# Kernel tuning notes

Measured on AMD Instinct MI355X. Metric: run time of the kernel, lower is better.

Reference implementation:

```python
import jax, jax.numpy as jnp
import numpy as np

FDIM = 512
NUM_HEADS = 8
FATT = FDIM // NUM_HEADS  # 64


def setup_inputs() -> dict:
    key = jax.random.key(0)
    ks = jax.random.split(key, 8)
    Nx, Np = 2048, 4096
    s = 0.05
    return {
        "fx_in": jax.random.normal(ks[0], (Nx, FDIM), jnp.float32),
        "fp_in": jax.random.normal(ks[1], (1, Np, FDIM), jnp.float32),
        "Wembd": jax.random.normal(ks[2], (NUM_HEADS, FATT, FDIM), jnp.float32) * s,
        "bembd": jax.random.normal(ks[3], (NUM_HEADS, FATT), jnp.float32) * s,
        "Wfc": jax.random.normal(ks[4], (NUM_HEADS, FATT, 2 * FATT), jnp.float32) * s,
        "bfc": jax.random.normal(ks[5], (NUM_HEADS, FATT), jnp.float32) * s,
        "Wout": jax.random.normal(ks[6], (FDIM, FATT * NUM_HEADS), jnp.float32) * s,
        "bout": jax.random.normal(ks[7], (FDIM,), jnp.float32) * s,
    }


def reference(fx_in, fp_in, Wembd, bembd, Wfc, bfc, Wout, bout):
    # fx_in: [Nx, F]; fp_in: [1, Np, F] -> squeeze leading dim
    fp0 = fp_in[0]
    Nx = fx_in.shape[0]
    d = jnp.sqrt(jnp.asarray(FATT, fx_in.dtype))
    # per-head embedding of concatenated [fx; fp]: [H, Nx+Np, e]
    f = jnp.concatenate([fx_in, fp0], axis=0)
    femb = jnp.einsum('nf,hef->hne', f, Wembd) + bembd[:, None, :]
    fx, fp = femb[:, :Nx], femb[:, Nx:]          # [H,Nx,e], [H,Np,e]
    # attention weights (dropout is identity in eval)
    scores = jnp.einsum('hxe,hpe->hxp', fx, fp) / d
    w = jax.nn.softmax(scores, axis=2)            # [H,Nx,Np]
    # gather + concat + per-head fuse MLP
    fa_att = jnp.einsum('hxp,hpe->hxe', w, fp)    # [H,Nx,e]
    fa = jnp.concatenate([fa_att, fx], axis=2)    # [H,Nx,2e]
    fa = jax.nn.relu(jnp.einsum('hxc,hec->hxe', fa, Wfc) + bfc[:, None, :])
    fa = jnp.transpose(fa, (1, 0, 2)).reshape(Nx, -1)  # [Nx, H*e]
    fx_out = jax.nn.relu(fx_in + fa @ Wout.T + bout)
    w_out = jnp.transpose(w, (1, 0, 2))           # [Nx, H, Np]
    return fx_out, w_out
```

## Files before the change

### kernel.cpp

```cpp
#include <hip/hip_runtime.h>

typedef unsigned short ushort_t;
using frag_ab = __attribute__((ext_vector_type(8))) short;
using f32x4   = __attribute__((ext_vector_type(4))) float;
using u32x4   = __attribute__((ext_vector_type(4))) unsigned int;
using u32x2   = __attribute__((ext_vector_type(2))) unsigned int;

#define FDIM 512
#define NH 8
#define FATT 64
#define NX 2048
#define NP 4096
#define NTOT 6144

__device__ __forceinline__ ushort_t f2bf(float f) {
    unsigned u = __float_as_uint(f);
    u = (u + 0x7FFFu + ((u >> 16) & 1u)) >> 16;
    return (ushort_t)u;
}
__device__ __forceinline__ float bf2f(ushort_t s) {
    return __uint_as_float(((unsigned)s) << 16);
}
__device__ __forceinline__ unsigned pk2bf(float a, float b) {
    return (unsigned)f2bf(a) | ((unsigned)f2bf(b) << 16);
}

__global__ __launch_bounds__(256) void k_prep(const float* __restrict__ fx,
                                              const float* __restrict__ fp,
                                              const float* __restrict__ We,
                                              const float* __restrict__ Wfc,
                                              const float* __restrict__ Wout,
                                              ushort_t* __restrict__ f_b,
                                              ushort_t* __restrict__ We_b,
                                              ushort_t* __restrict__ Wfc_b,
                                              ushort_t* __restrict__ Wout_b) {
    int i = blockIdx.x * 256 + threadIdx.x;
    int stride = gridDim.x * 256;
    const int NF4 = NTOT * FDIM / 4;
    const int NX4 = NX * FDIM / 4;
    for (int idx = i; idx < NF4; idx += stride) {
        float4 v = (idx < NX4) ? ((const float4*)fx)[idx]
                               : ((const float4*)fp)[idx - NX4];
        ushort4 o;
        o.x = f2bf(v.x); o.y = f2bf(v.y); o.z = f2bf(v.z); o.w = f2bf(v.w);
        ((ushort4*)f_b)[idx] = o;
    }
    const int NW4 = FDIM * FDIM / 4;
    for (int idx = i; idx < NW4; idx += stride) {
        float4 v = ((const float4*)We)[idx];
        ushort4 o;
        o.x = f2bf(v.x); o.y = f2bf(v.y); o.z = f2bf(v.z); o.w = f2bf(v.w);
        ((ushort4*)We_b)[idx] = o;
    }
    const int NFC4 = NH * FATT * 2 * FATT / 4;
    for (int idx = i; idx < NFC4; idx += stride) {
        float4 v = ((const float4*)Wfc)[idx];
        ushort4 o;
        o.x = f2bf(v.x); o.y = f2bf(v.y); o.z = f2bf(v.z); o.w = f2bf(v.w);
        ((ushort4*)Wfc_b)[idx] = o;
    }
    for (int idx = i; idx < NW4; idx += stride) {
        float4 v = ((const float4*)Wout)[idx];
        ushort4 o;
        o.x = f2bf(v.x); o.y = f2bf(v.y); o.z = f2bf(v.z); o.w = f2bf(v.w);
        ((ushort4*)Wout_b)[idx] = o;
    }
}

__global__ __launch_bounds__(256) void k_embed(const ushort_t* __restrict__ f_b,
                                               const ushort_t* __restrict__ We_b,
                                               const float* __restrict__ bembd,
                                               ushort_t* __restrict__ femb_b,
                                               ushort_t* __restrict__ fpT_b,
                                               ushort_t* __restrict__ facat_b) {
    int tid = threadIdx.x;
    int wv = tid >> 6, lane = tid & 63;
    int g = lane >> 4, c = lane & 15;
    int m0 = blockIdx.x * 64 + wv * 16;
    int o0 = blockIdx.y * 64;

    f32x4 acc[4] = {};
    const ushort_t* arow = f_b + (size_t)(m0 + c) * FDIM + g * 8;
#pragma unroll 4
    for (int ks = 0; ks < FDIM; ks += 32) {
        frag_ab a = *(const frag_ab*)(arow + ks);
#pragma unroll
        for (int t = 0; t < 4; ++t) {
            const ushort_t* brow = We_b + (size_t)(o0 + t * 16 + c) * FDIM + ks + g * 8;
            frag_ab b = *(const frag_ab*)brow;
            acc[t] = __builtin_amdgcn_mfma_f32_16x16x32_bf16(a, b, acc[t], 0, 0, 0);
        }
    }
#pragma unroll
    for (int t = 0; t < 4; ++t) {
        int o = o0 + t * 16 + c;
        int h = o >> 6, e = o & 63;
        float bia = bembd[o];
#pragma unroll
        for (int r = 0; r < 4; ++r) {
            int n = m0 + g * 4 + r;
            ushort_t v = f2bf(acc[t][r] + bia);
            femb_b[((size_t)h * NTOT + n) * FATT + e] = v;
            if (n >= NX) fpT_b[((size_t)h * FATT + e) * NP + (n - NX)] = v;
            else         facat_b[((size_t)h * NX + n) * 128 + 64 + e] = v;
        }
    }
}

__global__ __launch_bounds__(512) void k_attn_p1(const ushort_t* __restrict__ femb_b,
                                                 const ushort_t* __restrict__ fpT_b,
                                                 float* __restrict__ inv_sums,
                                                 ushort_t* __restrict__ facat_b) {
    int bid = blockIdx.x;
    int h  = bid & 7;
    int xb = bid >> 3;
    int tid = threadIdx.x;
    int wv = tid >> 6;
    int lane = tid & 63;
    int g = lane >> 4, c = lane & 15;

    __shared__ float lds_pv[64][68];
    __shared__ float lds_sum[64];
    __shared__ float lds_inv[64];

    const ushort_t* fxb = femb_b + (size_t)h * NTOT * FATT;
    const ushort_t* fpb = fxb + (size_t)NX * FATT;
    const ushort_t* fTb = fpT_b + (size_t)h * FATT * NP;

    frag_ab bx0_0, bx0_1, bx1_0, bx1_1, bx2_0, bx2_1, bx3_0, bx3_1;
    {
        const ushort_t* b0 = fxb + (size_t)(xb * 64 + 0 * 16 + c) * FATT + g * 8;
        const ushort_t* b1 = fxb + (size_t)(xb * 64 + 1 * 16 + c) * FATT + g * 8;
        const ushort_t* b2 = fxb + (size_t)(xb * 64 + 2 * 16 + c) * FATT + g * 8;
        const ushort_t* b3 = fxb + (size_t)(xb * 64 + 3 * 16 + c) * FATT + g * 8;
        bx0_0 = *(const frag_ab*)b0;  bx0_1 = *(const frag_ab*)(b0 + 32);
        bx1_0 = *(const frag_ab*)b1;  bx1_1 = *(const frag_ab*)(b1 + 32);
        bx2_0 = *(const frag_ab*)b2;  bx2_1 = *(const frag_ab*)(b2 + 32);
        bx3_0 = *(const frag_ab*)b3;  bx3_1 = *(const frag_ab*)(b3 + 32);
    }

    f32x4 pacc[4][4] = {};
    float rsum[4] = {0.f, 0.f, 0.f, 0.f};
    const int p0 = wv * 512;

    for (int ps = p0; ps < p0 + 512; ps += 16) {
        const ushort_t* ar = fpb + (size_t)(ps + c) * FATT + g * 8;
        frag_ab a0 = *(const frag_ab*)ar;
        frag_ab a1 = *(const frag_ab*)(ar + 32);
        frag_ab pb[4];
#pragma unroll
        for (int xg = 0; xg < 4; ++xg) {
            frag_ab q0 = (xg == 0) ? bx0_0 : (xg == 1) ? bx1_0 : (xg == 2) ? bx2_0 : bx3_0;
            frag_ab q1 = (xg == 0) ? bx0_1 : (xg == 1) ? bx1_1 : (xg == 2) ? bx2_1 : bx3_1;
            f32x4 s = {};
            s = __builtin_amdgcn_mfma_f32_16x16x32_bf16(a0, q0, s, 0, 0, 0);
            s = __builtin_amdgcn_mfma_f32_16x16x32_bf16(a1, q1, s, 0, 0, 0);
            float e0 = __expf(s[0] * 0.125f);
            float e1 = __expf(s[1] * 0.125f);
            float e2 = __expf(s[2] * 0.125f);
            float e3 = __expf(s[3] * 0.125f);
            rsum[xg] += (e0 + e1) + (e2 + e3);
            u32x4 bw;
            bw[0] = pk2bf(e0, e1);
            bw[1] = pk2bf(e2, e3);
            bw[2] = 0u;
            bw[3] = 0u;
            pb[xg] = __builtin_bit_cast(frag_ab, bw);
        }
#pragma unroll
        for (int t2 = 0; t2 < 4; ++t2) {
            const ushort_t* vr = fTb + (size_t)(t2 * 16 + c) * NP + ps + g * 4;
            u32x2 vl = *(const u32x2*)vr;
            u32x4 aw;
            aw[0] = vl[0];
            aw[1] = vl[1];
            aw[2] = 0u;
            aw[3] = 0u;
            frag_ab va = __builtin_bit_cast(frag_ab, aw);
#pragma unroll
            for (int xg = 0; xg < 4; ++xg)
                pacc[xg][t2] = __builtin_amdgcn_mfma_f32_16x16x32_bf16(va, pb[xg], pacc[xg][t2], 0, 0, 0);
        }
    }

#pragma unroll
    for (int xg = 0; xg < 4; ++xg) {
        rsum[xg] += __shfl_xor(rsum[xg], 16);
        rsum[xg] += __shfl_xor(rsum[xg], 32);
    }

    for (int w = 0; w < 8; ++w) {
        if (wv == w) {
            if (w == 0) {
                if (lane < 16) {
#pragma unroll
                    for (int xg = 0; xg < 4; ++xg) lds_sum[xg * 16 + c] = rsum[xg];
                }
#pragma unroll
                for (int xg = 0; xg < 4; ++xg)
#pragma unroll
                    for (int t2 = 0; t2 < 4; ++t2)
                        *(f32x4*)&lds_pv[xg * 16 + c][t2 * 16 + 4 * g] = pacc[xg][t2];
            } else {
                if (lane < 16) {
#pragma unroll
                    for (int xg = 0; xg < 4; ++xg) lds_sum[xg * 16 + c] += rsum[xg];
                }
#pragma unroll
                for (int xg = 0; xg < 4; ++xg)
#pragma unroll
                    for (int t2 = 0; t2 < 4; ++t2) {
                        f32x4 cur = *(const f32x4*)&lds_pv[xg * 16 + c][t2 * 16 + 4 * g];
                        cur += pacc[xg][t2];
                        *(f32x4*)&lds_pv[xg * 16 + c][t2 * 16 + 4 * g] = cur;
                    }
            }
        }
        __syncthreads();
    }
    if (tid < 64) {
        float inv = 1.f / lds_sum[tid];
        lds_inv[tid] = inv;
        inv_sums[(size_t)h * NX + xb * 64 + tid] = inv;
    }
    __syncthreads();

    {
        int row = tid >> 3;
        int e0 = (tid & 7) * 8;
        float inv = lds_inv[row];
        u32x4 o;
#pragma unroll
        for (int j = 0; j < 4; ++j)
            o[j] = pk2bf(lds_pv[row][e0 + 2 * j] * inv, lds_pv[row][e0 + 2 * j + 1] * inv);
        *(u32x4*)&facat_b[((size_t)h * NX + xb * 64 + row) * 128 + e0] = o;
    }
}

__global__ __launch_bounds__(256) void k_wout(const ushort_t* __restrict__ femb_b,
                                              const float* __restrict__ inv_sums,
                                              float* __restrict__ w_out) {
    int bid = blockIdx.x;
    int h  = bid & 7;
    int wv = threadIdx.x >> 6;
    int t1 = (bid >> 3) * 4 + wv;
    int xt = t1 & 127;
    int sl = t1 >> 7;
    int lane = threadIdx.x & 63;
    int g = lane >> 4, c = lane & 15;

    __shared__ float lds[4][16][132];

    const ushort_t* fxb = femb_b + (size_t)h * NTOT * FATT;
    const ushort_t* fpb = fxb + (size_t)NX * FATT;

    const ushort_t* brow = fxb + (size_t)(xt * 16 + c) * FATT + g * 8;
    frag_ab b0 = *(const frag_ab*)(brow);
    frag_ab b1 = *(const frag_ab*)(brow + 32);
    float inv_c = inv_sums[(size_t)h * NX + xt * 16 + c];

    const int p0 = sl * 512;
    for (int chunk = 0; chunk < 512; chunk += 128) {
#pragma unroll
        for (int pt = 0; pt < 8; ++pt) {
            int ps = p0 + chunk + pt * 16;
            const ushort_t* arow = fpb + (size_t)(ps + c) * FATT + g * 8;
            f32x4 s = {};
            s = __builtin_amdgcn_mfma_f32_16x16x32_bf16(*(const frag_ab*)arow, b0, s, 0, 0, 0);
            s = __builtin_amdgcn_mfma_f32_16x16x32_bf16(*(const frag_ab*)(arow + 32), b1, s, 0, 0, 0);
            f32x4 ev;
            ev[0] = __expf(s[0] * 0.125f) * inv_c;
            ev[1] = __expf(s[1] * 0.125f) * inv_c;
            ev[2] = __expf(s[2] * 0.125f) * inv_c;
            ev[3] = __expf(s[3] * 0.125f) * inv_c;
            int sw = (pt * 16 + g * 4) ^ ((c & 7) << 4);
            *(f32x4*)&lds[wv][c][sw] = ev;
        }
        __syncthreads();
#pragma unroll
        for (int row = 0; row < 16; ++row) {
            int pi = lane * 2;
            int swr = pi ^ ((row & 7) << 4);
            float2 v = *(const float2*)&lds[wv][row][swr];
            float* dst = w_out + ((size_t)(xt * 16 + row) * NH + h) * NP + p0 + chunk + pi;
            *(float2*)dst = v;
        }
        __syncthreads();
    }
}

__global__ __launch_bounds__(256) void k_fc(const ushort_t* __restrict__ facat_b,
                                            const ushort_t* __restrict__ Wfc_b,
                                            const float* __restrict__ bfc,
                                            ushort_t* __restrict__ fcout_b) {
    int tid = threadIdx.x;
    int wv = tid >> 6, lane = tid & 63;
    int g = lane >> 4, c = lane & 15;
    int x0 = blockIdx.x * 64 + wv * 16;
    int h = blockIdx.y;

    const ushort_t* A = facat_b + ((size_t)h * NX + x0 + c) * 128 + g * 8;
    const ushort_t* B = Wfc_b + (size_t)h * FATT * 128;

    f32x4 acc[4] = {};
#pragma unroll
    for (int ks = 0; ks < 128; ks += 32) {
        frag_ab a = *(const frag_ab*)(A + ks);
#pragma unroll
        for (int t = 0; t < 4; ++t) {
            frag_ab b = *(const frag_ab*)(B + (size_t)(t * 16 + c) * 128 + ks + g * 8);
            acc[t] = __builtin_amdgcn_mfma_f32_16x16x32_bf16(a, b, acc[t], 0, 0, 0);
        }
    }
#pragma unroll
    for (int t = 0; t < 4; ++t) {
        int e = t * 16 + c;
        float bia = bfc[h * FATT + e];
#pragma unroll
        for (int r = 0; r < 4; ++r) {
            int x = x0 + g * 4 + r;
            fcout_b[(size_t)x * FDIM + h * FATT + e] = f2bf(fmaxf(acc[t][r] + bia, 0.f));
        }
    }
}

__global__ __launch_bounds__(256) void k_out(const float* __restrict__ fx_in,
                                             const ushort_t* __restrict__ fcout_b,
                                             const ushort_t* __restrict__ Wout_b,
                                             const float* __restrict__ bout,
                                             float* __restrict__ out) {
    int tid = threadIdx.x;
    int wv = tid >> 6, lane = tid & 63;
    int g = lane >> 4, c = lane & 15;
    int x0 = blockIdx.x * 64 + wv * 16;
    int o0 = blockIdx.y * 64;

    f32x4 acc[4] = {};
    const ushort_t* A = fcout_b + (size_t)(x0 + c) * FDIM + g * 8;
#pragma unroll 4
    for (int ks = 0; ks < FDIM; ks += 32) {
        frag_ab a = *(const frag_ab*)(A + ks);
#pragma unroll
        for (int t = 0; t < 4; ++t) {
            frag_ab b = *(const frag_ab*)(Wout_b + (size_t)(o0 + t * 16 + c) * FDIM + ks + g * 8);
            acc[t] = __builtin_amdgcn_mfma_f32_16x16x32_bf16(a, b, acc[t], 0, 0, 0);
        }
    }
#pragma unroll
    for (int t = 0; t < 4; ++t) {
        int f = o0 + t * 16 + c;
        float bia = bout[f];
#pragma unroll
        for (int r = 0; r < 4; ++r) {
            int x = x0 + g * 4 + r;
            float v = acc[t][r] + bia + fx_in[(size_t)x * FDIM + f];
            out[(size_t)x * FDIM + f] = fmaxf(v, 0.f);
        }
    }
}

extern "C" void kernel_launch(void* const* d_in, const int* in_sizes, int n_in,
                              void* d_out, int out_size, void* d_ws, size_t ws_size,
                              hipStream_t stream) {
    const float* fx_in = (const float*)d_in[0];
    const float* fp_in = (const float*)d_in[1];
    const float* Wembd = (const float*)d_in[2];
    const float* bembd = (const float*)d_in[3];
    const float* Wfc   = (const float*)d_in[4];
    const float* bfc   = (const float*)d_in[5];
    const float* Wout  = (const float*)d_in[6];
    const float* bout  = (const float*)d_in[7];

    float* out   = (float*)d_out;
    float* w_out = out + (size_t)NX * FDIM;

    ushort_t* f_b     = (ushort_t*)d_ws;
    ushort_t* We_b    = f_b + (size_t)NTOT * FDIM;
    ushort_t* femb_b  = We_b + (size_t)FDIM * FDIM;
    ushort_t* fpT_b   = femb_b + (size_t)NH * NTOT * FATT;
    ushort_t* facat_b = fpT_b + (size_t)NH * FATT * NP;
    ushort_t* fcout_b = facat_b + (size_t)NH * NX * 128;
    ushort_t* Wfc_b   = fcout_b + (size_t)NX * FDIM;
    ushort_t* Wout_b  = Wfc_b + (size_t)NH * FATT * 2 * FATT;
    float*    inv_sums= (float*)(Wout_b + (size_t)FDIM * FDIM);

    k_prep   <<<1024, 256, 0, stream>>>(fx_in, fp_in, Wembd, Wfc, Wout,
                                        f_b, We_b, Wfc_b, Wout_b);
    k_embed  <<<dim3(96, 8), 256, 0, stream>>>(f_b, We_b, bembd, femb_b, fpT_b, facat_b);
    k_attn_p1<<<256, 512, 0, stream>>>(femb_b, fpT_b, inv_sums, facat_b);
    k_wout   <<<2048, 256, 0, stream>>>(femb_b, inv_sums, w_out);
    k_fc     <<<dim3(32, 8), 256, 0, stream>>>(facat_b, Wfc_b, bfc, fcout_b);
    k_out    <<<dim3(32, 8), 256, 0, stream>>>(fx_in, fcout_b, Wout_b, bout, out);
}
```

Before: 191.6 us.

## Double attention block waves and retile w_out kernel for fragment reuse

The attention pass-1 kernel now launches 16 waves per block instead of 8, each covering 256 key positions, which halves the serial p-loop per wave and adds more parallelism. The w_out kernel is retiled so each wave holds four x-row fragments and reuses eight preloaded key fragments across them, and it drops the __syncthreads barriers because each wave uses its own LDS slice. This aims to cut repeated global loads of fp fragments and barrier stalls. The costs are higher register pressure in both kernels and a longer serial cross-wave reduction in pass 1.

After: 197.7 us. 1.03x slower.

```diff
diff --git a/kernel.cpp b/kernel.cpp
--- a/kernel.cpp
+++ b/kernel.cpp
@@ -107,10 +107,10 @@
     }
 }
 
-__global__ __launch_bounds__(512) void k_attn_p1(const ushort_t* __restrict__ femb_b,
-                                                 const ushort_t* __restrict__ fpT_b,
-                                                 float* __restrict__ inv_sums,
-                                                 ushort_t* __restrict__ facat_b) {
+__global__ __launch_bounds__(1024) void k_attn_p1(const ushort_t* __restrict__ femb_b,
+                                                  const ushort_t* __restrict__ fpT_b,
+                                                  float* __restrict__ inv_sums,
+                                                  ushort_t* __restrict__ facat_b) {
     int bid = blockIdx.x;
     int h  = bid & 7;
     int xb = bid >> 3;
@@ -141,9 +141,9 @@
 
     f32x4 pacc[4][4] = {};
     float rsum[4] = {0.f, 0.f, 0.f, 0.f};
-    const int p0 = wv * 512;
-
-    for (int ps = p0; ps < p0 + 512; ps += 16) {
+    const int p0 = wv * 256;
+
+    for (int ps = p0; ps < p0 + 256; ps += 16) {
         const ushort_t* ar = fpb + (size_t)(ps + c) * FATT + g * 8;
         frag_ab a0 = *(const frag_ab*)ar;
         frag_ab a1 = *(const frag_ab*)(ar + 32);
@@ -189,7 +189,7 @@
         rsum[xg] += __shfl_xor(rsum[xg], 32);
     }
 
-    for (int w = 0; w < 8; ++w) {
+    for (int w = 0; w < 16; ++w) {
         if (wv == w) {
             if (w == 0) {
                 if (lane < 16) {
@@ -225,7 +225,7 @@
     }
     __syncthreads();
 
-    {
+    if (tid < 512) {
         int row = tid >> 3;
         int e0 = (tid & 7) * 8;
         float inv = lds_inv[row];
@@ -241,12 +241,13 @@
                                               const float* __restrict__ inv_sums,
                                               float* __restrict__ w_out) {
     int bid = blockIdx.x;
-    int h  = bid & 7;
-    int wv = threadIdx.x >> 6;
-    int t1 = (bid >> 3) * 4 + wv;
-    int xt = t1 & 127;
-    int sl = t1 >> 7;
-    int lane = threadIdx.x & 63;
+    int h    = bid & 7;
+    int rest = bid >> 3;
+    int xb   = rest & 31;
+    int sl   = rest >> 5;
+    int tid = threadIdx.x;
+    int wv = tid >> 6;
+    int lane = tid & 63;
     int g = lane >> 4, c = lane & 15;
 
     __shared__ float lds[4][16][132];
@@ -254,38 +255,50 @@
     const ushort_t* fxb = femb_b + (size_t)h * NTOT * FATT;
     const ushort_t* fpb = fxb + (size_t)NX * FATT;
 
-    const ushort_t* brow = fxb + (size_t)(xt * 16 + c) * FATT + g * 8;
-    frag_ab b0 = *(const frag_ab*)(brow);
-    frag_ab b1 = *(const frag_ab*)(brow + 32);
-    float inv_c = inv_sums[(size_t)h * NX + xt * 16 + c];
-
-    const int p0 = sl * 512;
-    for (int chunk = 0; chunk < 512; chunk += 128) {
+    frag_ab q0[4], q1[4];
+    float inv[4];
+#pragma unroll
+    for (int xg = 0; xg < 4; ++xg) {
+        const ushort_t* b = fxb + (size_t)(xb * 64 + xg * 16 + c) * FATT + g * 8;
+        q0[xg] = *(const frag_ab*)b;
+        q1[xg] = *(const frag_ab*)(b + 32);
+        inv[xg] = inv_sums[(size_t)h * NX + xb * 64 + xg * 16 + c];
+    }
+
+    const int p_base = sl * 1024 + wv * 256;
+    for (int chunk = 0; chunk < 2; ++chunk) {
+        int pc = p_base + chunk * 128;
+        frag_ab af0[8], af1[8];
 #pragma unroll
         for (int pt = 0; pt < 8; ++pt) {
-            int ps = p0 + chunk + pt * 16;
-            const ushort_t* arow = fpb + (size_t)(ps + c) * FATT + g * 8;
-            f32x4 s = {};
-            s = __builtin_amdgcn_mfma_f32_16x16x32_bf16(*(const frag_ab*)arow, b0, s, 0, 0, 0);
-            s = __builtin_amdgcn_mfma_f32_16x16x32_bf16(*(const frag_ab*)(arow + 32), b1, s, 0, 0, 0);
-            f32x4 ev;
-            ev[0] = __expf(s[0] * 0.125f) * inv_c;
-            ev[1] = __expf(s[1] * 0.125f) * inv_c;
-            ev[2] = __expf(s[2] * 0.125f) * inv_c;
-            ev[3] = __expf(s[3] * 0.125f) * inv_c;
-            int sw = (pt * 16 + g * 4) ^ ((c & 7) << 4);
-            *(f32x4*)&lds[wv][c][sw] = ev;
-        }
-        __syncthreads();
-#pragma unroll
-        for (int row = 0; row < 16; ++row) {
-            int pi = lane * 2;
-            int swr = pi ^ ((row & 7) << 4);
-            float2 v = *(const float2*)&lds[wv][row][swr];
-            float* dst = w_out + ((size_t)(xt * 16 + row) * NH + h) * NP + p0 + chunk + pi;
-            *(float2*)dst = v;
-        }
-        __syncthreads();
+            const ushort_t* ar = fpb + (size_t)(pc + pt * 16 + c) * FATT + g * 8;
+            af0[pt] = *(const frag_ab*)ar;
+            af1[pt] = *(const frag_ab*)(ar + 32);
+        }
+#pragma unroll
+        for (int xg = 0; xg < 4; ++xg) {
+#pragma unroll
+            for (int pt = 0; pt < 8; ++pt) {
+                f32x4 s = {};
+                s = __builtin_amdgcn_mfma_f32_16x16x32_bf16(af0[pt], q0[xg], s, 0, 0, 0);
+                s = __builtin_amdgcn_mfma_f32_16x16x32_bf16(af1[pt], q1[xg], s, 0, 0, 0);
+                f32x4 ev;
+                ev[0] = __expf(s[0] * 0.125f) * inv[xg];
+                ev[1] = __expf(s[1] * 0.125f) * inv[xg];
+                ev[2] = __expf(s[2] * 0.125f) * inv[xg];
+                ev[3] = __expf(s[3] * 0.125f) * inv[xg];
+                int sw = (pt * 16 + g * 4) ^ ((c & 7) << 4);
+                *(f32x4*)&lds[wv][c][sw] = ev;
+            }
+#pragma unroll
+            for (int row = 0; row < 16; ++row) {
+                int pi = lane * 2;
+                int swr = pi ^ ((row & 7) << 4);
+                float2 v = *(const float2*)&lds[wv][row][swr];
+                float* dst = w_out + ((size_t)(xb * 64 + xg * 16 + row) * NH + h) * NP + pc + pi;
+                *(float2*)dst = v;
+            }
+        }
     }
 }
 
@@ -387,8 +400,8 @@
     k_prep   <<<1024, 256, 0, stream>>>(fx_in, fp_in, Wembd, Wfc, Wout,
                                         f_b, We_b, Wfc_b, Wout_b);
     k_embed  <<<dim3(96, 8), 256, 0, stream>>>(f_b, We_b, bembd, femb_b, fpT_b, facat_b);
-    k_attn_p1<<<256, 512, 0, stream>>>(femb_b, fpT_b, inv_sums, facat_b);
-    k_wout   <<<2048, 256, 0, stream>>>(femb_b, inv_sums, w_out);
+    k_attn_p1<<<256, 1024, 0, stream>>>(femb_b, fpT_b, inv_sums, facat_b);
+    k_wout   <<<1024, 256, 0, stream>>>(femb_b, inv_sums, w_out);
     k_fc     <<<dim3(32, 8), 256, 0, stream>>>(facat_b, Wfc_b, bfc, fcout_b);
     k_out    <<<dim3(32, 8), 256, 0, stream>>>(fx_in, fcout_b, Wout_b, bout, out);
 }
```
